# Kernel tuning notes

Hardware: AMD Instinct MI355X
Metric: run time of the kernel (lower is better)

## Reference

```python
import jax, jax.numpy as jnp
import numpy as np

N = 50000
NEG_SLOPE = 0.2
EPS = 1e-16


def gat_conv(x, src, dst, W, att_src, att_dst, bias, concat):
    H, C = att_src.shape
    xw = (x @ W).reshape(N, H, C)                      # [N,H,C]
    a_src = jnp.sum(xw * att_src, axis=-1)             # [N,H]
    a_dst = jnp.sum(xw * att_dst, axis=-1)             # [N,H]
    e = a_src[src] + a_dst[dst]                        # [E,H]
    e = jnp.where(e > 0, e, NEG_SLOPE * e)             # LeakyReLU(0.2)
    # segment softmax over edges grouped by destination node
    m = jax.ops.segment_max(e, dst, num_segments=N)    # [N,H]
    m = jnp.where(jnp.isfinite(m), m, 0.0)
    ex = jnp.exp(e - m[dst])
    s = jax.ops.segment_sum(ex, dst, num_segments=N)   # [N,H]
    alpha = ex / (s[dst] + EPS)                        # [E,H]
    msg = xw[src] * alpha[:, :, None]                  # [E,H,C]
    out = jax.ops.segment_sum(msg, dst, num_segments=N)  # [N,H,C]
    out = out.reshape(N, H * C) if concat else out.mean(axis=1)
    return out + bias


def setup_inputs() -> dict:
    key = jax.random.key(0)
    ks = jax.random.split(key, 12)
    E = 1_600_000
    return {
        "x": jax.random.normal(ks[0], (N, 128), jnp.float32),
        "edge_index": jax.random.randint(ks[1], (2, E), 0, N, jnp.int32),
        "W1": jax.random.normal(ks[2], (128, 128), jnp.float32) * 0.1,
        "att_src1": jax.random.normal(ks[3], (4, 32), jnp.float32) * 0.1,
        "att_dst1": jax.random.normal(ks[4], (4, 32), jnp.float32) * 0.1,
        "b1": jax.random.normal(ks[5], (128,), jnp.float32) * 0.1,
        "bn_gamma": jnp.ones((128,), jnp.float32),
        "bn_beta": jnp.zeros((128,), jnp.float32),
        "bn_mean": jnp.zeros((128,), jnp.float32),
        "bn_var": jnp.ones((128,), jnp.float32),
        "W2": jax.random.normal(ks[6], (128, 64), jnp.float32) * 0.1,
        "att_src2": jax.random.normal(ks[7], (1, 64), jnp.float32) * 0.1,
        "att_dst2": jax.random.normal(ks[8], (1, 64), jnp.float32) * 0.1,
        "b2": jax.random.normal(ks[9], (64,), jnp.float32) * 0.1,
    }


def reference(x, edge_index, W1, att_src1, att_dst1, b1,
              bn_gamma, bn_beta, bn_mean, bn_var,
              W2, att_src2, att_dst2, b2):
    # PyG GATConv adds self-loops by default
    loops = jnp.arange(N, dtype=edge_index.dtype)
    src = jnp.concatenate([edge_index[0], loops])
    dst = jnp.concatenate([edge_index[1], loops])
    h = gat_conv(x, src, dst, W1, att_src1, att_dst1, b1, concat=True)
    # BatchNorm1d in eval mode (running stats), then ELU; dropout is identity in eval
    h = (h - bn_mean) * jax.lax.rsqrt(bn_var + 1e-5) * bn_gamma + bn_beta
    h = jax.nn.elu(h)
    out = gat_conv(h, src, dst, W2, att_src2, att_dst2, b2, concat=False)
    return out
```

## Files before the change

### kernel.cpp

```cpp
#include <hip/hip_runtime.h>
#include <hip/hip_bf16.h>
#include <hip/hip_fp16.h>


#define NNODES 50000
#define NODE_SHIFT 7
#define BKTS ((NNODES + 127) / 128)
#define CHUNK 4096
#define CAP 8192

typedef __bf16 bf16x8 __attribute__((ext_vector_type(8)));
typedef float f32x4 __attribute__((ext_vector_type(4)));

__global__ void wpack_k(const float* __restrict__ W1, const float* __restrict__ W2,
                        __hip_bfloat16* __restrict__ Wp1, __hip_bfloat16* __restrict__ Wp2) {
    constexpr int TOT1 = 8 * 4 * 64;
    constexpr int TOT2 = 4 * 4 * 64;
    int i = blockIdx.x * blockDim.x + threadIdx.x;
    if (i < TOT1) {
        int l = i & 63, s = (i >> 6) & 3, t = i >> 8;
        int quad = l >> 4, col = l & 15;
#pragma unroll
        for (int j = 0; j < 8; ++j) {
            float f = W1[(s * 32 + quad * 8 + j) * 128 + t * 16 + col];
            Wp1[(size_t)i * 8 + j] = __float2bfloat16(f);
        }
    } else if (i < TOT1 + TOT2) {
        int i2 = i - TOT1;
        int l = i2 & 63, s = (i2 >> 6) & 3, t = i2 >> 8;
        int quad = l >> 4, col = l & 15;
#pragma unroll
        for (int j = 0; j < 8; ++j) {
            float f = W2[(s * 32 + quad * 8 + j) * 64 + t * 16 + col];
            Wp2[(size_t)i2 * 8 + j] = __float2bfloat16(f);
        }
    }
}

template <int COLS, bool IN_BF16>
__global__ __launch_bounds__(256) void gemm_mfma_k(
    const void* __restrict__ Xv, const __hip_bfloat16* __restrict__ Wp,
    __hip_bfloat16* __restrict__ Y,
    const float* __restrict__ atts, const float* __restrict__ attd,
    float* __restrict__ a_s, float* __restrict__ a_d, int M) {
    constexpr int NH = (COLS == 128) ? 4 : 1;
    const int wid = threadIdx.x >> 6, lane = threadIdx.x & 63;
    const int tile = blockIdx.x * 4 + wid;
    if (tile * 16 >= M) return;
    const int quad = lane >> 4, col = lane & 15;
    const int row = tile * 16 + col;

    bf16x8 afr[4];
    if (IN_BF16) {
        const __hip_bfloat16* X = (const __hip_bfloat16*)Xv;
#pragma unroll
        for (int s = 0; s < 4; ++s)
            afr[s] = *(const bf16x8*)(X + (size_t)row * 128 + s * 32 + quad * 8);
    } else {
        const float* X = (const float*)Xv;
#pragma unroll
        for (int s = 0; s < 4; ++s) {
            const float4* p = (const float4*)(X + (size_t)row * 128 + s * 32 + quad * 8);
            float4 f0 = p[0], f1 = p[1];
            afr[s][0] = (__bf16)f0.x; afr[s][1] = (__bf16)f0.y;
            afr[s][2] = (__bf16)f0.z; afr[s][3] = (__bf16)f0.w;
            afr[s][4] = (__bf16)f1.x; afr[s][5] = (__bf16)f1.y;
            afr[s][6] = (__bf16)f1.z; afr[s][7] = (__bf16)f1.w;
        }
    }

    float asp[4][NH], adp[4][NH];
#pragma unroll
    for (int r = 0; r < 4; ++r)
#pragma unroll
        for (int h = 0; h < NH; ++h) { asp[r][h] = 0.f; adp[r][h] = 0.f; }

    const bf16x8* Wp8 = (const bf16x8*)Wp;
#pragma unroll
    for (int t = 0; t < COLS / 16; ++t) {
        f32x4 acc = {0.f, 0.f, 0.f, 0.f};
#pragma unroll
        for (int s = 0; s < 4; ++s) {
            bf16x8 bfr = Wp8[(t * 4 + s) * 64 + lane];
            acc = __builtin_amdgcn_mfma_f32_16x16x32_bf16(afr[s], bfr, acc, 0, 0, 0);
        }
        const int gc = t * 16 + col;
        const int h = (NH == 4) ? (t >> 1) : 0;
        const float ws = atts[gc], wd = attd[gc];
#pragma unroll
        for (int r = 0; r < 4; ++r) {
            asp[r][h] += acc[r] * ws;
            adp[r][h] += acc[r] * wd;
            Y[(size_t)(tile * 16 + quad * 4 + r) * COLS + gc] = __float2bfloat16(acc[r]);
        }
    }

#pragma unroll
    for (int off = 1; off <= 8; off <<= 1) {
#pragma unroll
        for (int r = 0; r < 4; ++r)
#pragma unroll
            for (int h = 0; h < NH; ++h) {
                asp[r][h] += __shfl_xor(asp[r][h], off);
                adp[r][h] += __shfl_xor(adp[r][h], off);
            }
    }
    if (col == 0) {
#pragma unroll
        for (int r = 0; r < 4; ++r) {
            int rw = tile * 16 + quad * 4 + r;
#pragma unroll
            for (int h = 0; h < NH; ++h) {
                a_s[rw * NH + h] = asp[r][h];
                a_d[rw * NH + h] = adp[r][h];
            }
        }
    }
}

__global__ __launch_bounds__(256) void hist_bucket_k(const int* __restrict__ edst,
                                                     int E, int Etot, int NB,
                                                     int* __restrict__ g_hist) {
    __shared__ int h[BKTS];
    for (int b = threadIdx.x; b < BKTS; b += 256) h[b] = 0;
    __syncthreads();
    const int e0 = blockIdx.x * CHUNK;
    const int e1 = min(e0 + CHUNK, Etot);
    for (int i = e0 + threadIdx.x; i < e1; i += 256) {
        int d = (i < E) ? edst[i] : (i - E);
        atomicAdd(&h[d >> NODE_SHIFT], 1);
    }
    __syncthreads();
    for (int b = threadIdx.x; b < BKTS; b += 256)
        g_hist[b * NB + blockIdx.x] = h[b];
}

__global__ __launch_bounds__(256) void scan1_k(const int* __restrict__ cnt,
                                               int* __restrict__ partial,
                                               int* __restrict__ bsum, int Nn) {
    __shared__ int sA[256];
    int i = blockIdx.x * 256 + threadIdx.x;
    sA[threadIdx.x] = (i < Nn) ? cnt[i] : 0;
    __syncthreads();
    for (int off = 1; off < 256; off <<= 1) {
        int u = (threadIdx.x >= off) ? sA[threadIdx.x - off] : 0;
        __syncthreads();
        sA[threadIdx.x] += u;
        __syncthreads();
    }
    if (i < Nn) partial[i] = sA[threadIdx.x];
    if (threadIdx.x == 255) bsum[blockIdx.x] = sA[255];
}

__global__ __launch_bounds__(256) void scan2_k(int* __restrict__ bsum, int nb) {
    __shared__ int sA[256];
    const int t = threadIdx.x;
    int carry = 0;
    for (int base = 0; base < nb; base += 256) {
        int i = base + t;
        sA[t] = (i < nb) ? bsum[i] : 0;
        __syncthreads();
        for (int off = 1; off < 256; off <<= 1) {
            int u = (t >= off) ? sA[t - off] : 0;
            __syncthreads();
            sA[t] += u;
            __syncthreads();
        }
        if (i < nb) bsum[i] = sA[t] + carry;
        carry += sA[255];
        __syncthreads();
    }
}

__global__ void scan3_k(const int* __restrict__ partial, const int* __restrict__ bsum,
                        int* __restrict__ out, int Nn) {
    int i = blockIdx.x * 256 + threadIdx.x;
    if (i >= Nn) return;
    int b = blockIdx.x;
    int off = (b == 0) ? 0 : bsum[b - 1];
    out[i + 1] = partial[i] + off;
    if (i == 0) out[0] = 0;
}

__global__ __launch_bounds__(256) void scatter_bucket_k(
    const int* __restrict__ esrc, const int* __restrict__ edst,
    int E, int Etot, int NB, const int* __restrict__ scanned,
    unsigned int* __restrict__ gbucket) {
    __shared__ int cur[BKTS];
    for (int b = threadIdx.x; b < BKTS; b += 256)
        cur[b] = scanned[b * NB + blockIdx.x];
    __syncthreads();
    const int e0 = blockIdx.x * CHUNK;
    const int e1 = min(e0 + CHUNK, Etot);
    for (int i = e0 + threadIdx.x; i < e1; i += 256) {
        int s, d;
        if (i < E) { s = esrc[i]; d = edst[i]; }
        else       { s = i - E;   d = i - E; }
        int pos = atomicAdd(&cur[d >> NODE_SHIFT], 1);
        gbucket[pos] = ((unsigned)(d & 127) << 16) | (unsigned)s;
    }
}

__global__ __launch_bounds__(256) void finalize_k(
    const unsigned int* __restrict__ gbucket, const int* __restrict__ scanned,
    int NB, int Etot, unsigned short* __restrict__ ssrc,
    int* __restrict__ rowptr, int Nn) {
    const int b = blockIdx.x;
    const int base = scanned[b * NB];
    const int end = (b + 1 < BKTS) ? scanned[(b + 1) * NB] : Etot;
    const int cnt = end - base;
    const int t = threadIdx.x;

    __shared__ unsigned int keys[CAP];
    __shared__ int hist[128], sA[128], cur[128];

    for (int i = t; i < cnt; i += 256) keys[i] = gbucket[base + i];
    if (t < 128) hist[t] = 0;
    __syncthreads();
    for (int i = t; i < cnt; i += 256) atomicAdd(&hist[keys[i] >> 16], 1);
    __syncthreads();
    if (t < 128) sA[t] = hist[t];
    __syncthreads();
    for (int off = 1; off < 128; off <<= 1) {
        int u = 0;
        if (t < 128 && t >= off) u = sA[t - off];
        __syncthreads();
        if (t < 128) sA[t] += u;
        __syncthreads();
    }
    if (t < 128) {
        int excl = sA[t] - hist[t];
        cur[t] = excl;
        int node = b * 128 + t;
        if (node <= Nn) rowptr[node] = base + excl;
    }
    __syncthreads();
    for (int i = t; i < cnt; i += 256) {
        unsigned k = keys[i];
        int p = atomicAdd(&cur[k >> 16], 1);
        ssrc[base + p] = (unsigned short)(k & 0xFFFFu);
    }
}

__global__ __launch_bounds__(256) void agg1_k(
    const int* __restrict__ rowptr, const unsigned short* __restrict__ ssrc,
    const __hip_bfloat16* __restrict__ xw,
    const float* __restrict__ a_s, const float* __restrict__ a_d,
    const float* __restrict__ bias,
    const float* __restrict__ gamma, const float* __restrict__ beta,
    const float* __restrict__ mean, const float* __restrict__ var,
    __hip_bfloat16* __restrict__ out, int Nn) {
    int n = (blockIdx.x * blockDim.x + threadIdx.x) >> 6;
    int lane = threadIdx.x & 63;
    if (n >= Nn) return;
    const int r0 = rowptr[n];
    const int deg = rowptr[n + 1] - r0;
    const int g = lane >> 4, q = lane & 15;
    const int c0 = q * 8;
    const int h = q >> 2;
    const float adh = a_d[n * 4 + h];

    float ssum = 0.f;
    float acc[8];
#pragma unroll
    for (int k = 0; k < 8; ++k) acc[k] = 0.f;

    int j = 0;
    for (; j + 16 <= deg; j += 16) {
        int sid[4];
#pragma unroll
        for (int b = 0; b < 4; ++b) sid[b] = ssrc[r0 + j + b * 4 + g];
        float as[4];
        bf16x8 f[4];
#pragma unroll
        for (int b = 0; b < 4; ++b) {
            as[b] = a_s[sid[b] * 4 + h];
            f[b] = *(const bf16x8*)(xw + (size_t)sid[b] * 128 + c0);
        }
#pragma unroll
        for (int b = 0; b < 4; ++b) {
            float e = as[b] + adh;
            e = (e > 0.f) ? e : 0.2f * e;
            float p = __expf(e);
            ssum += p;
#pragma unroll
            for (int k = 0; k < 8; ++k) acc[k] += p * (float)f[b][k];
        }
    }
    for (; j < deg; j += 4) {
        int jj = j + g;
        bool ok = jj < deg;
        int sid = ssrc[r0 + (ok ? jj : j)];
        float e = a_s[sid * 4 + h] + adh;
        e = (e > 0.f) ? e : 0.2f * e;
        float p = ok ? __expf(e) : 0.f;
        ssum += p;
        bf16x8 f = *(const bf16x8*)(xw + (size_t)sid * 128 + c0);
#pragma unroll
        for (int k = 0; k < 8; ++k) acc[k] += p * (float)f[k];
    }
#pragma unroll
    for (int off = 16; off <= 32; off <<= 1) {
        ssum += __shfl_xor(ssum, off);
#pragma unroll
        for (int k = 0; k < 8; ++k) acc[k] += __shfl_xor(acc[k], off);
    }
    if (g == 0) {
        const float inv = 1.f / (ssum + 1e-16f);
        bf16x8 o;
#pragma unroll
        for (int k = 0; k < 8; ++k) {
            int c = c0 + k;
            float v = acc[k] * inv + bias[c];
            v = (v - mean[c]) * rsqrtf(var[c] + 1e-5f) * gamma[c] + beta[c];
            v = (v > 0.f) ? v : (__expf(v) - 1.f);
            o[k] = (__bf16)v;
        }
        *(bf16x8*)(out + (size_t)n * 128 + c0) = o;
    }
}

__global__ __launch_bounds__(256) void agg2_k(
    const int* __restrict__ rowptr, const unsigned short* __restrict__ ssrc,
    const __hip_bfloat16* __restrict__ xw,
    const float* __restrict__ a_s, const float* __restrict__ a_d,
    const float* __restrict__ bias, float* __restrict__ out, int Nn) {
    int n = (blockIdx.x * blockDim.x + threadIdx.x) >> 6;
    int lane = threadIdx.x & 63;
    if (n >= Nn) return;
    const int r0 = rowptr[n];
    const int deg = rowptr[n + 1] - r0;
    const int g = lane >> 3, q = lane & 7;
    const int c0 = q * 8;
    const float adn = a_d[n];

    float ssum = 0.f;
    float acc[8];
#pragma unroll
    for (int k = 0; k < 8; ++k) acc[k] = 0.f;

    int j = 0;
    for (; j + 32 <= deg; j += 32) {
        int sid[4];
#pragma unroll
        for (int b = 0; b < 4; ++b) sid[b] = ssrc[r0 + j + b * 8 + g];
        float as[4];
        bf16x8 f[4];
#pragma unroll
        for (int b = 0; b < 4; ++b) {
            as[b] = a_s[sid[b]];
            f[b] = *(const bf16x8*)(xw + (size_t)sid[b] * 64 + c0);
        }
#pragma unroll
        for (int b = 0; b < 4; ++b) {
            float e = as[b] + adn;
            e = (e > 0.f) ? e : 0.2f * e;
            float p = __expf(e);
            ssum += p;
#pragma unroll
            for (int k = 0; k < 8; ++k) acc[k] += p * (float)f[b][k];
        }
    }
    for (; j < deg; j += 8) {
        int jj = j + g;
        bool ok = jj < deg;
        int sid = ssrc[r0 + (ok ? jj : j)];
        float e = a_s[sid] + adn;
        e = (e > 0.f) ? e : 0.2f * e;
        float p = ok ? __expf(e) : 0.f;
        ssum += p;
        bf16x8 f = *(const bf16x8*)(xw + (size_t)sid * 64 + c0);
#pragma unroll
        for (int k = 0; k < 8; ++k) acc[k] += p * (float)f[k];
    }
#pragma unroll
    for (int off = 8; off <= 32; off <<= 1) {
        ssum += __shfl_xor(ssum, off);
#pragma unroll
        for (int k = 0; k < 8; ++k) acc[k] += __shfl_xor(acc[k], off);
    }
    if (g == 0) {
        const float inv = 1.f / (ssum + 1e-16f);
        float4 o0, o1;
        o0.x = acc[0] * inv + bias[c0];
        o0.y = acc[1] * inv + bias[c0 + 1];
        o0.z = acc[2] * inv + bias[c0 + 2];
        o0.w = acc[3] * inv + bias[c0 + 3];
        o1.x = acc[4] * inv + bias[c0 + 4];
        o1.y = acc[5] * inv + bias[c0 + 5];
        o1.z = acc[6] * inv + bias[c0 + 6];
        o1.w = acc[7] * inv + bias[c0 + 7];
        *(float4*)(out + (size_t)n * 64 + c0) = o0;
        *(float4*)(out + (size_t)n * 64 + c0 + 4) = o1;
    }
}

extern "C" void kernel_launch(void* const* d_in, const int* in_sizes, int n_in,
                              void* d_out, int out_size, void* d_ws, size_t ws_size,
                              hipStream_t stream) {
    const float* x     = (const float*)d_in[0];
    const int*   ei    = (const int*)d_in[1];
    const float* W1    = (const float*)d_in[2];
    const float* as1   = (const float*)d_in[3];
    const float* ad1   = (const float*)d_in[4];
    const float* b1    = (const float*)d_in[5];
    const float* gamma = (const float*)d_in[6];
    const float* beta  = (const float*)d_in[7];
    const float* mean  = (const float*)d_in[8];
    const float* var   = (const float*)d_in[9];
    const float* W2    = (const float*)d_in[10];
    const float* as2   = (const float*)d_in[11];
    const float* ad2   = (const float*)d_in[12];
    const float* b2    = (const float*)d_in[13];
    float* out = (float*)d_out;

    const int N = NNODES;
    const int E = in_sizes[1] / 2;
    const int Etot = E + N;
    const int* esrc = ei;
    const int* edst = ei + E;

    const int NB = (Etot + CHUNK - 1) / CHUNK;
    const int flatN = BKTS * NB;

    char* w = (char*)d_ws;
    __hip_bfloat16* xw1 = (__hip_bfloat16*)w; w += (size_t)N * 128 * 2;
    __hip_bfloat16* hbuf = (__hip_bfloat16*)w; w += (size_t)N * 128 * 2;
    __hip_bfloat16* xw2 = (__hip_bfloat16*)w; w += (size_t)N * 64 * 2;
    float* a_s1 = (float*)w; w += (size_t)N * 4 * 4;
    float* a_d1 = (float*)w; w += (size_t)N * 4 * 4;
    unsigned int* gbucket = (unsigned int*)w; w += (size_t)Etot * 4 + 16;
    int* g_hist  = (int*)w;  w += (size_t)flatN * 4 + 16;
    int* partial = (int*)w;  w += (size_t)flatN * 4 + 16;
    int* scanned = (int*)w;  w += (size_t)(flatN + 4) * 4 + 16;
    int* bsum    = (int*)w;  w += 4096;
    int* rowptr  = (int*)w;  w += (size_t)(N + 8) * 4;
    unsigned short* ssrc_s = (unsigned short*)w; w += (size_t)Etot * 2 + 16;
    __hip_bfloat16* wp1 = (__hip_bfloat16*)w; w += 8 * 4 * 64 * 8 * 2;
    __hip_bfloat16* wp2 = (__hip_bfloat16*)w; w += 4 * 4 * 64 * 8 * 2;
    float* a_s2 = a_s1; float* a_d2 = a_d1;

    const int TB = 256;
    const int nb2 = (flatN + 255) / 256;
    const int aggBlocks  = (N + 3) / 4;
    const int gemmBlocks = (N / 16 + 3) / 4;

    wpack_k<<<(8 * 4 * 64 + 4 * 4 * 64 + TB - 1) / TB, TB, 0, stream>>>(W1, W2, wp1, wp2);

    hist_bucket_k<<<NB, TB, 0, stream>>>(edst, E, Etot, NB, g_hist);
    scan1_k<<<nb2, TB, 0, stream>>>(g_hist, partial, bsum, flatN);
    scan2_k<<<1, TB, 0, stream>>>(bsum, nb2);
    scan3_k<<<nb2, TB, 0, stream>>>(partial, bsum, scanned, flatN);
    scatter_bucket_k<<<NB, TB, 0, stream>>>(esrc, edst, E, Etot, NB, scanned, gbucket);
    finalize_k<<<BKTS, TB, 0, stream>>>(gbucket, scanned, NB, Etot, ssrc_s, rowptr, N);

    gemm_mfma_k<128, false><<<gemmBlocks, TB, 0, stream>>>(x, wp1, xw1,
                                                           as1, ad1, a_s1, a_d1, N);
    agg1_k<<<aggBlocks, TB, 0, stream>>>(rowptr, ssrc_s, xw1, a_s1, a_d1,
                                         b1, gamma, beta, mean, var, hbuf, N);

    gemm_mfma_k<64, true><<<gemmBlocks, TB, 0, stream>>>(hbuf, wp2, xw2,
                                                         as2, ad2, a_s2, a_d2, N);
    agg2_k<<<aggBlocks, TB, 0, stream>>>(rowptr, ssrc_s, xw2, a_s2, a_d2, b2, out, N);
}
```

Measured before the change: 256.5 us.

## Replace per-block bucket histogram scan with global atomic bucket totals

The edge bucketing pipeline now accumulates per-bucket totals with global atomics and scans only 391 bucket totals in a single small kernel, instead of scanning a full bucket-by-block matrix across three kernels. Scatter blocks recompute their local histogram and reserve ranges through atomic cursors, and the weight packing is folded into the histogram launch. This removes several launches and scan passes but adds a memset, a second read of dst in scatter, and makes edge order within a bucket nondeterministic.

```diff
diff --git a/kernel.cpp b/kernel.cpp
--- a/kernel.cpp
+++ b/kernel.cpp
@@ -12,28 +12,142 @@
 typedef __bf16 bf16x8 __attribute__((ext_vector_type(8)));
 typedef float f32x4 __attribute__((ext_vector_type(4)));
 
-__global__ void wpack_k(const float* __restrict__ W1, const float* __restrict__ W2,
-                        __hip_bfloat16* __restrict__ Wp1, __hip_bfloat16* __restrict__ Wp2) {
-    constexpr int TOT1 = 8 * 4 * 64;
-    constexpr int TOT2 = 4 * 4 * 64;
-    int i = blockIdx.x * blockDim.x + threadIdx.x;
-    if (i < TOT1) {
-        int l = i & 63, s = (i >> 6) & 3, t = i >> 8;
-        int quad = l >> 4, col = l & 15;
-#pragma unroll
-        for (int j = 0; j < 8; ++j) {
-            float f = W1[(s * 32 + quad * 8 + j) * 128 + t * 16 + col];
-            Wp1[(size_t)i * 8 + j] = __float2bfloat16(f);
-        }
-    } else if (i < TOT1 + TOT2) {
-        int i2 = i - TOT1;
-        int l = i2 & 63, s = (i2 >> 6) & 3, t = i2 >> 8;
-        int quad = l >> 4, col = l & 15;
-#pragma unroll
-        for (int j = 0; j < 8; ++j) {
-            float f = W2[(s * 32 + quad * 8 + j) * 64 + t * 16 + col];
-            Wp2[(size_t)i2 * 8 + j] = __float2bfloat16(f);
-        }
+__global__ __launch_bounds__(256) void hist_wpack_k(
+    const int* __restrict__ edst, int E, int Etot, int NB,
+    int* __restrict__ btot,
+    const float* __restrict__ W1, const float* __restrict__ W2,
+    __hip_bfloat16* __restrict__ Wp1, __hip_bfloat16* __restrict__ Wp2) {
+    if ((int)blockIdx.x >= NB) {
+        constexpr int TOT1 = 8 * 4 * 64;
+        constexpr int TOT2 = 4 * 4 * 64;
+        int i = (blockIdx.x - NB) * 256 + threadIdx.x;
+        if (i < TOT1) {
+            int l = i & 63, s = (i >> 6) & 3, t = i >> 8;
+            int quad = l >> 4, col = l & 15;
+#pragma unroll
+            for (int j = 0; j < 8; ++j) {
+                float f = W1[(s * 32 + quad * 8 + j) * 128 + t * 16 + col];
+                Wp1[(size_t)i * 8 + j] = __float2bfloat16(f);
+            }
+        } else if (i < TOT1 + TOT2) {
+            int i2 = i - TOT1;
+            int l = i2 & 63, s = (i2 >> 6) & 3, t = i2 >> 8;
+            int quad = l >> 4, col = l & 15;
+#pragma unroll
+            for (int j = 0; j < 8; ++j) {
+                float f = W2[(s * 32 + quad * 8 + j) * 64 + t * 16 + col];
+                Wp2[(size_t)i2 * 8 + j] = __float2bfloat16(f);
+            }
+        }
+        return;
+    }
+    __shared__ int h[BKTS];
+    for (int b = threadIdx.x; b < BKTS; b += 256) h[b] = 0;
+    __syncthreads();
+    const int e0 = blockIdx.x * CHUNK;
+    const int e1 = min(e0 + CHUNK, Etot);
+    for (int i = e0 + threadIdx.x; i < e1; i += 256) {
+        int d = (i < E) ? edst[i] : (i - E);
+        atomicAdd(&h[d >> NODE_SHIFT], 1);
+    }
+    __syncthreads();
+    for (int b = threadIdx.x; b < BKTS; b += 256)
+        if (h[b] > 0) atomicAdd(&btot[b], h[b]);
+}
+
+__global__ __launch_bounds__(256) void scan_small_k(
+    const int* __restrict__ btot, int* __restrict__ base,
+    int* __restrict__ cursor, int nb) {
+    __shared__ int sA[256];
+    const int t = threadIdx.x;
+    int carry = 0;
+    for (int b0 = 0; b0 < nb; b0 += 256) {
+        int i = b0 + t;
+        int v = (i < nb) ? btot[i] : 0;
+        sA[t] = v;
+        __syncthreads();
+        for (int off = 1; off < 256; off <<= 1) {
+            int u = (t >= off) ? sA[t - off] : 0;
+            __syncthreads();
+            sA[t] += u;
+            __syncthreads();
+        }
+        if (i < nb) {
+            int incl = sA[t] + carry;
+            int excl = incl - v;
+            base[i] = excl;
+            cursor[i] = excl;
+            if (i == nb - 1) base[nb] = incl;
+        }
+        carry += sA[255];
+        __syncthreads();
+    }
+}
+
+__global__ __launch_bounds__(256) void scatter_bucket_k(
+    const int* __restrict__ esrc, const int* __restrict__ edst,
+    int E, int Etot, int* __restrict__ cursor,
+    unsigned int* __restrict__ gbucket) {
+    __shared__ int h[BKTS], rb[BKTS], lcur[BKTS];
+    for (int b = threadIdx.x; b < BKTS; b += 256) { h[b] = 0; lcur[b] = 0; }
+    __syncthreads();
+    const int e0 = blockIdx.x * CHUNK;
+    const int e1 = min(e0 + CHUNK, Etot);
+    for (int i = e0 + threadIdx.x; i < e1; i += 256) {
+        int d = (i < E) ? edst[i] : (i - E);
+        atomicAdd(&h[d >> NODE_SHIFT], 1);
+    }
+    __syncthreads();
+    for (int b = threadIdx.x; b < BKTS; b += 256)
+        if (h[b] > 0) rb[b] = atomicAdd(&cursor[b], h[b]);
+    __syncthreads();
+    for (int i = e0 + threadIdx.x; i < e1; i += 256) {
+        int s, d;
+        if (i < E) { s = esrc[i]; d = edst[i]; }
+        else       { s = i - E;   d = i - E; }
+        int k = d >> NODE_SHIFT;
+        int pos = rb[k] + atomicAdd(&lcur[k], 1);
+        gbucket[pos] = ((unsigned)(d & 127) << 16) | (unsigned)s;
+    }
+}
+
+__global__ __launch_bounds__(256) void finalize_k(
+    const unsigned int* __restrict__ gbucket, const int* __restrict__ base,
+    unsigned short* __restrict__ ssrc, int* __restrict__ rowptr, int Nn) {
+    const int b = blockIdx.x;
+    const int bbase = base[b];
+    const int end = base[b + 1];
+    const int cnt = end - bbase;
+    const int t = threadIdx.x;
+
+    __shared__ unsigned int keys[CAP];
+    __shared__ int hist[128], sA[128], cur[128];
+
+    for (int i = t; i < cnt; i += 256) keys[i] = gbucket[bbase + i];
+    if (t < 128) hist[t] = 0;
+    __syncthreads();
+    for (int i = t; i < cnt; i += 256) atomicAdd(&hist[keys[i] >> 16], 1);
+    __syncthreads();
+    if (t < 128) sA[t] = hist[t];
+    __syncthreads();
+    for (int off = 1; off < 128; off <<= 1) {
+        int u = 0;
+        if (t < 128 && t >= off) u = sA[t - off];
+        __syncthreads();
+        if (t < 128) sA[t] += u;
+        __syncthreads();
+    }
+    if (t < 128) {
+        int excl = sA[t] - hist[t];
+        cur[t] = excl;
+        int node = b * 128 + t;
+        if (node <= Nn) rowptr[node] = bbase + excl;
+    }
+    __syncthreads();
+    for (int i = t; i < cnt; i += 256) {
+        unsigned k = keys[i];
+        int p = atomicAdd(&cur[k >> 16], 1);
+        ssrc[bbase + p] = (unsigned short)(k & 0xFFFFu);
     }
 }
 
@@ -115,130 +229,6 @@
                 a_d[rw * NH + h] = adp[r][h];
             }
         }
-    }
-}
-
-__global__ __launch_bounds__(256) void hist_bucket_k(const int* __restrict__ edst,
-                                                     int E, int Etot, int NB,
-                                                     int* __restrict__ g_hist) {
-    __shared__ int h[BKTS];
-    for (int b = threadIdx.x; b < BKTS; b += 256) h[b] = 0;
-    __syncthreads();
-    const int e0 = blockIdx.x * CHUNK;
-    const int e1 = min(e0 + CHUNK, Etot);
-    for (int i = e0 + threadIdx.x; i < e1; i += 256) {
-        int d = (i < E) ? edst[i] : (i - E);
-        atomicAdd(&h[d >> NODE_SHIFT], 1);
-    }
-    __syncthreads();
-    for (int b = threadIdx.x; b < BKTS; b += 256)
-        g_hist[b * NB + blockIdx.x] = h[b];
-}
-
-__global__ __launch_bounds__(256) void scan1_k(const int* __restrict__ cnt,
-                                               int* __restrict__ partial,
-                                               int* __restrict__ bsum, int Nn) {
-    __shared__ int sA[256];
-    int i = blockIdx.x * 256 + threadIdx.x;
-    sA[threadIdx.x] = (i < Nn) ? cnt[i] : 0;
-    __syncthreads();
-    for (int off = 1; off < 256; off <<= 1) {
-        int u = (threadIdx.x >= off) ? sA[threadIdx.x - off] : 0;
-        __syncthreads();
-        sA[threadIdx.x] += u;
-        __syncthreads();
-    }
-    if (i < Nn) partial[i] = sA[threadIdx.x];
-    if (threadIdx.x == 255) bsum[blockIdx.x] = sA[255];
-}
-
-__global__ __launch_bounds__(256) void scan2_k(int* __restrict__ bsum, int nb) {
-    __shared__ int sA[256];
-    const int t = threadIdx.x;
-    int carry = 0;
-    for (int base = 0; base < nb; base += 256) {
-        int i = base + t;
-        sA[t] = (i < nb) ? bsum[i] : 0;
-        __syncthreads();
-        for (int off = 1; off < 256; off <<= 1) {
-            int u = (t >= off) ? sA[t - off] : 0;
-            __syncthreads();
-            sA[t] += u;
-            __syncthreads();
-        }
-        if (i < nb) bsum[i] = sA[t] + carry;
-        carry += sA[255];
-        __syncthreads();
-    }
-}
-
-__global__ void scan3_k(const int* __restrict__ partial, const int* __restrict__ bsum,
-                        int* __restrict__ out, int Nn) {
-    int i = blockIdx.x * 256 + threadIdx.x;
-    if (i >= Nn) return;
-    int b = blockIdx.x;
-    int off = (b == 0) ? 0 : bsum[b - 1];
-    out[i + 1] = partial[i] + off;
-    if (i == 0) out[0] = 0;
-}
-
-__global__ __launch_bounds__(256) void scatter_bucket_k(
-    const int* __restrict__ esrc, const int* __restrict__ edst,
-    int E, int Etot, int NB, const int* __restrict__ scanned,
-    unsigned int* __restrict__ gbucket) {
-    __shared__ int cur[BKTS];
-    for (int b = threadIdx.x; b < BKTS; b += 256)
-        cur[b] = scanned[b * NB + blockIdx.x];
-    __syncthreads();
-    const int e0 = blockIdx.x * CHUNK;
-    const int e1 = min(e0 + CHUNK, Etot);
-    for (int i = e0 + threadIdx.x; i < e1; i += 256) {
-        int s, d;
-        if (i < E) { s = esrc[i]; d = edst[i]; }
-        else       { s = i - E;   d = i - E; }
-        int pos = atomicAdd(&cur[d >> NODE_SHIFT], 1);
-        gbucket[pos] = ((unsigned)(d & 127) << 16) | (unsigned)s;
-    }
-}
-
-__global__ __launch_bounds__(256) void finalize_k(
-    const unsigned int* __restrict__ gbucket, const int* __restrict__ scanned,
-    int NB, int Etot, unsigned short* __restrict__ ssrc,
-    int* __restrict__ rowptr, int Nn) {
-    const int b = blockIdx.x;
-    const int base = scanned[b * NB];
-    const int end = (b + 1 < BKTS) ? scanned[(b + 1) * NB] : Etot;
-    const int cnt = end - base;
-    const int t = threadIdx.x;
-
-    __shared__ unsigned int keys[CAP];
-    __shared__ int hist[128], sA[128], cur[128];
-
-    for (int i = t; i < cnt; i += 256) keys[i] = gbucket[base + i];
-    if (t < 128) hist[t] = 0;
-    __syncthreads();
-    for (int i = t; i < cnt; i += 256) atomicAdd(&hist[keys[i] >> 16], 1);
-    __syncthreads();
-    if (t < 128) sA[t] = hist[t];
-    __syncthreads();
-    for (int off = 1; off < 128; off <<= 1) {
-        int u = 0;
-        if (t < 128 && t >= off) u = sA[t - off];
-        __syncthreads();
-        if (t < 128) sA[t] += u;
-        __syncthreads();
-    }
-    if (t < 128) {
-        int excl = sA[t] - hist[t];
-        cur[t] = excl;
-        int node = b * 128 + t;
-        if (node <= Nn) rowptr[node] = base + excl;
-    }
-    __syncthreads();
-    for (int i = t; i < cnt; i += 256) {
-        unsigned k = keys[i];
-        int p = atomicAdd(&cur[k >> 16], 1);
-        ssrc[base + p] = (unsigned short)(k & 0xFFFFu);
     }
 }
 
@@ -421,7 +411,6 @@
     const int* edst = ei + E;
 
     const int NB = (Etot + CHUNK - 1) / CHUNK;
-    const int flatN = BKTS * NB;
 
     char* w = (char*)d_ws;
     __hip_bfloat16* xw1 = (__hip_bfloat16*)w; w += (size_t)N * 128 * 2;
@@ -430,29 +419,26 @@
     float* a_s1 = (float*)w; w += (size_t)N * 4 * 4;
     float* a_d1 = (float*)w; w += (size_t)N * 4 * 4;
     unsigned int* gbucket = (unsigned int*)w; w += (size_t)Etot * 4 + 16;
-    int* g_hist  = (int*)w;  w += (size_t)flatN * 4 + 16;
-    int* partial = (int*)w;  w += (size_t)flatN * 4 + 16;
-    int* scanned = (int*)w;  w += (size_t)(flatN + 4) * 4 + 16;
-    int* bsum    = (int*)w;  w += 4096;
-    int* rowptr  = (int*)w;  w += (size_t)(N + 8) * 4;
+    int* btot   = (int*)w;  w += (size_t)(BKTS + 4) * 4;
+    int* base   = (int*)w;  w += (size_t)(BKTS + 4) * 4;
+    int* cursor = (int*)w;  w += (size_t)(BKTS + 4) * 4;
+    int* rowptr = (int*)w;  w += (size_t)(N + 8) * 4;
     unsigned short* ssrc_s = (unsigned short*)w; w += (size_t)Etot * 2 + 16;
     __hip_bfloat16* wp1 = (__hip_bfloat16*)w; w += 8 * 4 * 64 * 8 * 2;
     __hip_bfloat16* wp2 = (__hip_bfloat16*)w; w += 4 * 4 * 64 * 8 * 2;
     float* a_s2 = a_s1; float* a_d2 = a_d1;
 
     const int TB = 256;
-    const int nb2 = (flatN + 255) / 256;
     const int aggBlocks  = (N + 3) / 4;
     const int gemmBlocks = (N / 16 + 3) / 4;
-
-    wpack_k<<<(8 * 4 * 64 + 4 * 4 * 64 + TB - 1) / TB, TB, 0, stream>>>(W1, W2, wp1, wp2);
-
-    hist_bucket_k<<<NB, TB, 0, stream>>>(edst, E, Etot, NB, g_hist);
-    scan1_k<<<nb2, TB, 0, stream>>>(g_hist, partial, bsum, flatN);
-    scan2_k<<<1, TB, 0, stream>>>(bsum, nb2);
-    scan3_k<<<nb2, TB, 0, stream>>>(partial, bsum, scanned, flatN);
-    scatter_bucket_k<<<NB, TB, 0, stream>>>(esrc, edst, E, Etot, NB, scanned, gbucket);
-    finalize_k<<<BKTS, TB, 0, stream>>>(gbucket, scanned, NB, Etot, ssrc_s, rowptr, N);
+    const int wpackBlocks = (8 * 4 * 64 + 4 * 4 * 64 + TB - 1) / TB;
+
+    hipMemsetAsync(btot, 0, (size_t)BKTS * 4, stream);
+    hist_wpack_k<<<NB + wpackBlocks, TB, 0, stream>>>(edst, E, Etot, NB, btot,
+                                                      W1, W2, wp1, wp2);
+    scan_small_k<<<1, TB, 0, stream>>>(btot, base, cursor, BKTS);
+    scatter_bucket_k<<<NB, TB, 0, stream>>>(esrc, edst, E, Etot, cursor, gbucket);
+    finalize_k<<<BKTS, TB, 0, stream>>>(gbucket, base, ssrc_s, rowptr, N);
 
     gemm_mfma_k<128, false><<<gemmBlocks, TB, 0, stream>>>(x, wp1, xw1,
                                                            as1, ad1, a_s1, a_d1, N);
```

New measurement: 273.3 us. 1.07x slower.

## Merge independent stages into shared launches via block-range dispatch

Applied to the files above, without the earlier changes.

Weight packing now runs as extra blocks of the histogram kernel, and the first-layer GEMM runs as extra blocks of the edge scatter kernel. Blocks pick their role from blockIdx. This removes two kernel launches and lets independent work fill the GPU at the same time. The cost is more register and LDS pressure in the combined kernels, since the shared-memory arrays and the GEMM registers now count toward the same kernel's occupancy.

```diff
diff --git a/kernel.cpp b/kernel.cpp
--- a/kernel.cpp
+++ b/kernel.cpp
@@ -12,40 +12,13 @@
 typedef __bf16 bf16x8 __attribute__((ext_vector_type(8)));
 typedef float f32x4 __attribute__((ext_vector_type(4)));
 
-__global__ void wpack_k(const float* __restrict__ W1, const float* __restrict__ W2,
-                        __hip_bfloat16* __restrict__ Wp1, __hip_bfloat16* __restrict__ Wp2) {
-    constexpr int TOT1 = 8 * 4 * 64;
-    constexpr int TOT2 = 4 * 4 * 64;
-    int i = blockIdx.x * blockDim.x + threadIdx.x;
-    if (i < TOT1) {
-        int l = i & 63, s = (i >> 6) & 3, t = i >> 8;
-        int quad = l >> 4, col = l & 15;
-#pragma unroll
-        for (int j = 0; j < 8; ++j) {
-            float f = W1[(s * 32 + quad * 8 + j) * 128 + t * 16 + col];
-            Wp1[(size_t)i * 8 + j] = __float2bfloat16(f);
-        }
-    } else if (i < TOT1 + TOT2) {
-        int i2 = i - TOT1;
-        int l = i2 & 63, s = (i2 >> 6) & 3, t = i2 >> 8;
-        int quad = l >> 4, col = l & 15;
-#pragma unroll
-        for (int j = 0; j < 8; ++j) {
-            float f = W2[(s * 32 + quad * 8 + j) * 64 + t * 16 + col];
-            Wp2[(size_t)i2 * 8 + j] = __float2bfloat16(f);
-        }
-    }
-}
-
 template <int COLS, bool IN_BF16>
-__global__ __launch_bounds__(256) void gemm_mfma_k(
-    const void* __restrict__ Xv, const __hip_bfloat16* __restrict__ Wp,
-    __hip_bfloat16* __restrict__ Y,
+__device__ __forceinline__ void gemm_body(
+    int tile, int lane, const void* __restrict__ Xv,
+    const __hip_bfloat16* __restrict__ Wp, __hip_bfloat16* __restrict__ Y,
     const float* __restrict__ atts, const float* __restrict__ attd,
     float* __restrict__ a_s, float* __restrict__ a_d, int M) {
     constexpr int NH = (COLS == 128) ? 4 : 1;
-    const int wid = threadIdx.x >> 6, lane = threadIdx.x & 63;
-    const int tile = blockIdx.x * 4 + wid;
     if (tile * 16 >= M) return;
     const int quad = lane >> 4, col = lane & 15;
     const int row = tile * 16 + col;
@@ -118,9 +91,35 @@
     }
 }
 
-__global__ __launch_bounds__(256) void hist_bucket_k(const int* __restrict__ edst,
-                                                     int E, int Etot, int NB,
-                                                     int* __restrict__ g_hist) {
+__global__ __launch_bounds__(256) void hist_wpack_k(
+    const int* __restrict__ edst, int E, int Etot, int NB,
+    int* __restrict__ g_hist,
+    const float* __restrict__ W1, const float* __restrict__ W2,
+    __hip_bfloat16* __restrict__ Wp1, __hip_bfloat16* __restrict__ Wp2) {
+    if ((int)blockIdx.x >= NB) {
+        constexpr int TOT1 = 8 * 4 * 64;
+        constexpr int TOT2 = 4 * 4 * 64;
+        int i = (blockIdx.x - NB) * 256 + threadIdx.x;
+        if (i < TOT1) {
+            int l = i & 63, s = (i >> 6) & 3, t = i >> 8;
+            int quad = l >> 4, col = l & 15;
+#pragma unroll
+            for (int j = 0; j < 8; ++j) {
+                float f = W1[(s * 32 + quad * 8 + j) * 128 + t * 16 + col];
+                Wp1[(size_t)i * 8 + j] = __float2bfloat16(f);
+            }
+        } else if (i < TOT1 + TOT2) {
+            int i2 = i - TOT1;
+            int l = i2 & 63, s = (i2 >> 6) & 3, t = i2 >> 8;
+            int quad = l >> 4, col = l & 15;
+#pragma unroll
+            for (int j = 0; j < 8; ++j) {
+                float f = W2[(s * 32 + quad * 8 + j) * 64 + t * 16 + col];
+                Wp2[(size_t)i2 * 8 + j] = __float2bfloat16(f);
+            }
+        }
+        return;
+    }
     __shared__ int h[BKTS];
     for (int b = threadIdx.x; b < BKTS; b += 256) h[b] = 0;
     __syncthreads();
@@ -182,10 +181,20 @@
     if (i == 0) out[0] = 0;
 }
 
-__global__ __launch_bounds__(256) void scatter_bucket_k(
+__global__ __launch_bounds__(256) void scatter_gemm_k(
     const int* __restrict__ esrc, const int* __restrict__ edst,
     int E, int Etot, int NB, const int* __restrict__ scanned,
-    unsigned int* __restrict__ gbucket) {
+    unsigned int* __restrict__ gbucket,
+    const float* __restrict__ X, const __hip_bfloat16* __restrict__ Wp1,
+    __hip_bfloat16* __restrict__ Y1,
+    const float* __restrict__ atts, const float* __restrict__ attd,
+    float* __restrict__ a_s, float* __restrict__ a_d, int M) {
+    if ((int)blockIdx.x >= NB) {
+        const int wid = threadIdx.x >> 6, lane = threadIdx.x & 63;
+        const int tile = (blockIdx.x - NB) * 4 + wid;
+        gemm_body<128, false>(tile, lane, X, Wp1, Y1, atts, attd, a_s, a_d, M);
+        return;
+    }
     __shared__ int cur[BKTS];
     for (int b = threadIdx.x; b < BKTS; b += 256)
         cur[b] = scanned[b * NB + blockIdx.x];
@@ -240,6 +249,17 @@
         int p = atomicAdd(&cur[k >> 16], 1);
         ssrc[base + p] = (unsigned short)(k & 0xFFFFu);
     }
+}
+
+template <int COLS, bool IN_BF16>
+__global__ __launch_bounds__(256) void gemm_mfma_k(
+    const void* __restrict__ Xv, const __hip_bfloat16* __restrict__ Wp,
+    __hip_bfloat16* __restrict__ Y,
+    const float* __restrict__ atts, const float* __restrict__ attd,
+    float* __restrict__ a_s, float* __restrict__ a_d, int M) {
+    const int wid = threadIdx.x >> 6, lane = threadIdx.x & 63;
+    const int tile = blockIdx.x * 4 + wid;
+    gemm_body<COLS, IN_BF16>(tile, lane, Xv, Wp, Y, atts, attd, a_s, a_d, M);
 }
 
 __global__ __launch_bounds__(256) void agg1_k(
@@ -444,18 +464,18 @@
     const int nb2 = (flatN + 255) / 256;
     const int aggBlocks  = (N + 3) / 4;
     const int gemmBlocks = (N / 16 + 3) / 4;
-
-    wpack_k<<<(8 * 4 * 64 + 4 * 4 * 64 + TB - 1) / TB, TB, 0, stream>>>(W1, W2, wp1, wp2);
-
-    hist_bucket_k<<<NB, TB, 0, stream>>>(edst, E, Etot, NB, g_hist);
+    const int wpackBlocks = (8 * 4 * 64 + 4 * 4 * 64 + TB - 1) / TB;
+
+    hist_wpack_k<<<NB + wpackBlocks, TB, 0, stream>>>(edst, E, Etot, NB, g_hist,
+                                                      W1, W2, wp1, wp2);
     scan1_k<<<nb2, TB, 0, stream>>>(g_hist, partial, bsum, flatN);
     scan2_k<<<1, TB, 0, stream>>>(bsum, nb2);
     scan3_k<<<nb2, TB, 0, stream>>>(partial, bsum, scanned, flatN);
-    scatter_bucket_k<<<NB, TB, 0, stream>>>(esrc, edst, E, Etot, NB, scanned, gbucket);
+    scatter_gemm_k<<<NB + gemmBlocks, TB, 0, stream>>>(
+        esrc, edst, E, Etot, NB, scanned, gbucket,
+        x, wp1, xw1, as1, ad1, a_s1, a_d1, N);
     finalize_k<<<BKTS, TB, 0, stream>>>(gbucket, scanned, NB, Etot, ssrc_s, rowptr, N);
 
-    gemm_mfma_k<128, false><<<gemmBlocks, TB, 0, stream>>>(x, wp1, xw1,
-                                                           as1, ad1, a_s1, a_d1, N);
     agg1_k<<<aggBlocks, TB, 0, stream>>>(rowptr, ssrc_s, xw1, a_s1, a_d1,
                                          b1, gamma, beta, mean, var, hbuf, N);
 
```

After: 252.8 us. Within noise of the previous version (-1.4%).
